# Kernel optimization log

Hardware: AMD Instinct MI355X
Metric: run time of the kernel (lower is better)

## Reference

```python
import jax, jax.numpy as jnp
import numpy as np
import math

N_FREQS = 32
MARGIN = 0.1
CHOUT = 270
POS_DIM = 2 * N_FREQS ** 2  # 2048


def fourier_emb(positions):
    # positions: [..., 2] in [0, 1]
    width = 1.0 + 2.0 * MARGIN
    p = (positions + MARGIN) / width
    f = jnp.arange(N_FREQS, dtype=p.dtype)
    two_pi = 2.0 * math.pi
    # phase[..., i, j] = 2*pi*(x*i + y*j)  -> flatten to [..., F*F]
    phase = two_pi * (p[..., 0][..., None, None] * f[:, None]
                      + p[..., 1][..., None, None] * f[None, :])
    phase = phase.reshape(*phase.shape[:-2], N_FREQS * N_FREQS)
    return jnp.concatenate([jnp.sin(phase), jnp.cos(phase)], axis=-1)  # [..., 2F^2]


def setup_inputs() -> dict:
    key = jax.random.key(0)
    k1, k2, k3 = jax.random.split(key, 3)
    B, C, T = 32, 273, 3000
    brain_data = jax.random.normal(k1, (B, C, T), dtype=jnp.float32)
    channel_layout = jax.random.uniform(k2, (B, C, 2), dtype=jnp.float32)
    heads = jax.random.normal(k3, (CHOUT, POS_DIM), dtype=jnp.float32) / POS_DIM ** 0.5
    return {"brain_data": brain_data, "channel_layout": channel_layout, "heads": heads}


def reference(brain_data, channel_layout, heads):
    # Eval mode: all channels valid, no dropout mask, zero score offset.
    emb = fourier_emb(channel_layout)                      # [B, C, D]
    scores = jnp.einsum('bcd,od->boc', emb, heads)         # [B, O, C]
    weights = jax.nn.softmax(scores, axis=-1)              # softmax over channels
    out = jnp.einsum('bct,boc->bot', brain_data, weights)  # [B, O, T]
    return out
```

## Files before the change

### kernel.cpp

```cpp
#include <hip/hip_runtime.h>
#include <hip/hip_bf16.h>
#include <hip/hip_fp16.h>

#define NB 32
#define NC 273
#define NT 3000
#define NO 270
#define ND 2048
#define CP 288

typedef _Float16 f16x8 __attribute__((ext_vector_type(8)));
typedef float f32x4 __attribute__((ext_vector_type(4)));

#define S_OFF 55296000UL
#define W_OFF 64730880UL
#define H_OFF 69707520UL

__device__ __forceinline__ unsigned short f2h_bits(float f) {
  _Float16 h = (_Float16)f;
  unsigned short u;
  __builtin_memcpy(&u, &h, 2);
  return u;
}

__global__ void heads_cvt_kernel(const float* __restrict__ heads,
                                 _Float16* __restrict__ hh) {
  const size_t idx = ((size_t)blockIdx.x * 256 + threadIdx.x) * 8;
  const float4 a = *reinterpret_cast<const float4*>(heads + idx);
  const float4 c = *reinterpret_cast<const float4*>(heads + idx + 4);
  f16x8 v;
  v[0] = (_Float16)a.x; v[1] = (_Float16)a.y; v[2] = (_Float16)a.z; v[3] = (_Float16)a.w;
  v[4] = (_Float16)c.x; v[5] = (_Float16)c.y; v[6] = (_Float16)c.z; v[7] = (_Float16)c.w;
  *reinterpret_cast<f16x8*>(hh + idx) = v;
}

__global__ void scores_kernel(const _Float16* __restrict__ hh,
                              const float* __restrict__ layout,
                              float* __restrict__ scores) {
  __shared__ _Float16 As[64][72];
  __shared__ _Float16 Bs[64][72];
  const int gid = blockIdx.x;
  const int tid = threadIdx.x;
  const int b = gid / 25;
  const int rem = gid % 25;
  const int o0 = (rem / 5) * 64;
  const int c0 = (rem % 5) * 64;
  const int lane = tid & 63, w = tid >> 6;
  const int wm = (w >> 1) * 32, wn = (w & 1) * 32;
  const int ln = lane & 15, quad = lane >> 4;
  const int sr = tid >> 2;
  const int sk = (tid & 3) * 16;

  const int ch = c0 + sr;
  float px = 0.f, py = 0.f;
  if (ch < NC) {
    const float inv = 1.0f / 1.2f;
    const float* lp = layout + ((size_t)b * NC + ch) * 2;
    px = (lp[0] + 0.1f) * inv;
    py = (lp[1] + 0.1f) * inv;
  }

  f32x4 acc[2][2] = {};

  for (int k0 = 0; k0 < ND; k0 += 64) {
    {
      const int o = o0 + sr;
      uint4 u0 = {0, 0, 0, 0}, u1 = {0, 0, 0, 0};
      if (o < NO) {
        const uint4* p = reinterpret_cast<const uint4*>(hh + (size_t)o * ND + k0 + sk);
        u0 = p[0]; u1 = p[1];
      }
      *reinterpret_cast<uint4*>(&As[sr][sk]) = u0;
      *reinterpret_cast<uint4*>(&As[sr][sk + 8]) = u1;
    }
    {
      const int kg = k0 + sk;
      const int dd = kg & 1023;
      const float base = px * (float)(dd >> 5) + py * (float)(dd & 31)
                       + ((kg < 1024) ? 0.0f : 0.25f);
      f16x8 h0, h1;
#pragma unroll
      for (int s = 0; s < 8; ++s) {
        float ph = base + py * (float)s;
        ph -= floorf(ph);
        h0[s] = (_Float16)__builtin_amdgcn_sinf(ph);
      }
#pragma unroll
      for (int s = 0; s < 8; ++s) {
        float ph = base + py * (float)(s + 8);
        ph -= floorf(ph);
        h1[s] = (_Float16)__builtin_amdgcn_sinf(ph);
      }
      *reinterpret_cast<f16x8*>(&Bs[sr][sk]) = h0;
      *reinterpret_cast<f16x8*>(&Bs[sr][sk + 8]) = h1;
    }
    __syncthreads();
#pragma unroll
    for (int ks = 0; ks < 64; ks += 32) {
      const int kf = ks + quad * 8;
      const f16x8 a0 = *reinterpret_cast<const f16x8*>(&As[wm + ln][kf]);
      const f16x8 a1 = *reinterpret_cast<const f16x8*>(&As[wm + 16 + ln][kf]);
      const f16x8 b0 = *reinterpret_cast<const f16x8*>(&Bs[wn + ln][kf]);
      const f16x8 b1 = *reinterpret_cast<const f16x8*>(&Bs[wn + 16 + ln][kf]);
      acc[0][0] = __builtin_amdgcn_mfma_f32_16x16x32_f16(a0, b0, acc[0][0], 0, 0, 0);
      acc[0][1] = __builtin_amdgcn_mfma_f32_16x16x32_f16(a0, b1, acc[0][1], 0, 0, 0);
      acc[1][0] = __builtin_amdgcn_mfma_f32_16x16x32_f16(a1, b0, acc[1][0], 0, 0, 0);
      acc[1][1] = __builtin_amdgcn_mfma_f32_16x16x32_f16(a1, b1, acc[1][1], 0, 0, 0);
    }
    __syncthreads();
  }

  float* sB = scores + (size_t)b * NO * NC;
#pragma unroll
  for (int i = 0; i < 2; ++i) {
    const int ob = o0 + wm + 16 * i + quad * 4;
#pragma unroll
    for (int j = 0; j < 2; ++j) {
      const int cc = c0 + wn + 16 * j + ln;
      if (cc >= NC) continue;
#pragma unroll
      for (int r = 0; r < 4; ++r) {
        const int o = ob + r;
        if (o < NO) sB[(size_t)o * NC + cc] = acc[i][j][r];
      }
    }
  }
}

__global__ void softmax_kernel(const float* __restrict__ sc,
                               _Float16* __restrict__ wq) {
  const int row = blockIdx.x * 4 + (threadIdx.x >> 6);
  const int lane = threadIdx.x & 63;
  const float* p = sc + (size_t)row * NC;
  _Float16* q = wq + (size_t)row * CP;
  float v[5];
  float m = -3.0e38f;
#pragma unroll
  for (int k = 0; k < 5; ++k) {
    const int c = lane + k * 64;
    v[k] = (c < NC) ? p[c] : -3.0e38f;
    m = fmaxf(m, v[k]);
  }
#pragma unroll
  for (int off = 32; off > 0; off >>= 1) m = fmaxf(m, __shfl_xor(m, off));
  float s = 0.f;
#pragma unroll
  for (int k = 0; k < 5; ++k) {
    v[k] = expf(v[k] - m);
    s += v[k];
  }
#pragma unroll
  for (int off = 32; off > 0; off >>= 1) s += __shfl_xor(s, off);
  const float r = 1.0f / s;
#pragma unroll
  for (int k = 0; k < 5; ++k) {
    const int c = lane + k * 64;
    if (c < NC) q[c] = (_Float16)(v[k] * r);
    else if (c < CP) q[c] = (_Float16)0.f;
  }
}

__global__ __launch_bounds__(256, 2) void out_kernel(
    const _Float16* __restrict__ wq,
    const float* __restrict__ brain,
    float* __restrict__ out) {
  __shared__ float raw[2][32][68];
  const int b = blockIdx.y;
  const int t0 = blockIdx.x * 64;
  const int tid = threadIdx.x;
  const int lane = tid & 63, w = tid >> 6;
  const int om = (w >> 1) * 32, tn = (w & 1) * 32;
  const int ln = lane & 15, quad = lane >> 4;

  const _Float16* Wb = wq + (size_t)b * NO * CP;

  const int cl = tid >> 3;
  const int tq = (tid & 7) * 4;
  const int tb = t0 + tq;
  const int wsw = (cl >> 3) << 4;
  const int ws0 = tq ^ wsw;
  const int ws1 = (tq + 32) ^ wsw;

  const int rc0 = (tn + ln) ^ (quad << 4);
  const int rc1 = (tn + 16 + ln) ^ (quad << 4);

  auto load_chunk = [&](int ci, float4& v0, float4& v1) {
    float4 z = {0.f, 0.f, 0.f, 0.f};
    v0 = z; v1 = z;
    const int c = ci * 32 + cl;
    if (c < NC) {
      const float* src = brain + ((size_t)b * NC + c) * NT + tb;
      if (tb + 35 < NT) {
        v0 = *reinterpret_cast<const float4*>(src);
        v1 = *reinterpret_cast<const float4*>(src + 32);
      } else {
        if (tb + 0 < NT) v0.x = src[0];
        if (tb + 1 < NT) v0.y = src[1];
        if (tb + 2 < NT) v0.z = src[2];
        if (tb + 3 < NT) v0.w = src[3];
        if (tb + 32 < NT) v1.x = src[32];
        if (tb + 33 < NT) v1.y = src[33];
        if (tb + 34 < NT) v1.z = src[34];
        if (tb + 35 < NT) v1.w = src[35];
      }
    }
  };

  auto store_raw = [&](int buf, const float4& v0, const float4& v1) {
    *reinterpret_cast<float4*>(&raw[buf][cl][ws0]) = v0;
    *reinterpret_cast<float4*>(&raw[buf][cl][ws1]) = v1;
  };

  auto load_a = [&](int s, f16x8 (&a)[10]) {
    const int kcol = s * 32 + quad * 8;
#pragma unroll
    for (int ot = 0; ot < 5; ++ot) {
      int r0 = ot * 64 + om + ln;      if (r0 > NO - 1) r0 = NO - 1;
      int r1 = ot * 64 + om + 16 + ln; if (r1 > NO - 1) r1 = NO - 1;
      a[2 * ot]     = *reinterpret_cast<const f16x8*>(Wb + (size_t)r0 * CP + kcol);
      a[2 * ot + 1] = *reinterpret_cast<const f16x8*>(Wb + (size_t)r1 * CP + kcol);
    }
  };

  f32x4 acc[5][2][2] = {};

  auto do_mfma = [&](const f16x8 (&a)[10], f16x8 b0, f16x8 b1) {
#pragma unroll
    for (int ot = 0; ot < 5; ++ot) {
      acc[ot][0][0] = __builtin_amdgcn_mfma_f32_16x16x32_f16(a[2*ot],   b0, acc[ot][0][0], 0, 0, 0);
      acc[ot][0][1] = __builtin_amdgcn_mfma_f32_16x16x32_f16(a[2*ot],   b1, acc[ot][0][1], 0, 0, 0);
      acc[ot][1][0] = __builtin_amdgcn_mfma_f32_16x16x32_f16(a[2*ot+1], b0, acc[ot][1][0], 0, 0, 0);
      acc[ot][1][1] = __builtin_amdgcn_mfma_f32_16x16x32_f16(a[2*ot+1], b1, acc[ot][1][1], 0, 0, 0);
    }
  };

  f16x8 aE[10], aO[10];
  float4 rA0, rA1, rB0, rB1;

  load_chunk(0, rA0, rA1);
  load_a(0, aE);
  load_chunk(1, rB0, rB1);
  store_raw(0, rA0, rA1);
  load_chunk(2, rA0, rA1);
  asm volatile("s_waitcnt lgkmcnt(0)" ::: "memory");
  __builtin_amdgcn_sched_barrier(0);
  __builtin_amdgcn_s_barrier();

#pragma unroll
  for (int s = 0; s < 9; ++s) {
    if (s < 8) {
      if (((s + 1) & 1) == 0) load_a(s + 1, aE); else load_a(s + 1, aO);
    }
    if (s < 8) {
      if (((s + 1) & 1) == 0) {
        store_raw(0, rA0, rA1);
        if (s < 6) load_chunk(s + 3, rA0, rA1);
      } else {
        store_raw(1, rB0, rB1);
        if (s < 6) load_chunk(s + 3, rB0, rB1);
      }
    }
    f16x8 b0, b1;
    {
      const float* rb = &raw[s & 1][0][0];
#pragma unroll
      for (int j = 0; j < 8; ++j) {
        const int row = quad * 8 + j;
        b0[j] = (_Float16)rb[row * 68 + rc0];
        b1[j] = (_Float16)rb[row * 68 + rc1];
      }
    }
    if (s < 8) {
      asm volatile("s_waitcnt lgkmcnt(0)" ::: "memory");
      __builtin_amdgcn_sched_barrier(0);
      __builtin_amdgcn_s_barrier();
    }
    if ((s & 1) == 0) do_mfma(aE, b0, b1); else do_mfma(aO, b0, b1);
  }

  float* oB = out + (size_t)b * NO * NT;
#pragma unroll
  for (int ot = 0; ot < 5; ++ot) {
#pragma unroll
    for (int i = 0; i < 2; ++i) {
      const int ob = ot * 64 + om + 16 * i + quad * 4;
#pragma unroll
      for (int j = 0; j < 2; ++j) {
        const int t = t0 + tn + 16 * j + ln;
        if (t >= NT) continue;
#pragma unroll
        for (int r = 0; r < 4; ++r) {
          const int o = ob + r;
          if (o < NO) oB[(size_t)o * NT + t] = acc[ot][i][j][r];
        }
      }
    }
  }
}

extern "C" void kernel_launch(void* const* d_in, const int* in_sizes, int n_in,
                              void* d_out, int out_size, void* d_ws, size_t ws_size,
                              hipStream_t stream) {
  const float* brain = (const float*)d_in[0];
  const float* layout = (const float*)d_in[1];
  const float* heads = (const float*)d_in[2];
  for (int i = 0; i < n_in; ++i) {
    if (in_sizes[i] == NB * NC * NT) brain = (const float*)d_in[i];
    else if (in_sizes[i] == NB * NC * 2) layout = (const float*)d_in[i];
    else if (in_sizes[i] == NO * ND) heads = (const float*)d_in[i];
  }
  float* out = (float*)d_out;

  float* scores = (float*)((char*)d_ws + S_OFF);
  _Float16* wq = (_Float16*)((char*)d_ws + W_OFF);
  _Float16* hh = (_Float16*)((char*)d_ws + H_OFF);

  heads_cvt_kernel<<<NO, 256, 0, stream>>>(heads, hh);
  scores_kernel<<<800, 256, 0, stream>>>(hh, layout, scores);
  softmax_kernel<<<(NB * NO) / 4, 256, 0, stream>>>(scores, wq);
  out_kernel<<<dim3(47, NB), 256, 0, stream>>>(wq, brain, out);
}
```

Baseline: 290.4 us.

## Stage full brain tile into LDS via direct global-to-LDS loads, drop pipeline

Replaces the double-buffered register-staged pipeline for the brain tile with a single bulk prefetch of all 288x64 floats into shared memory using global_load_lds (direct global-to-LDS DMA) with an XOR swizzle. The last channel is handled separately and the padding rows are zeroed. After one barrier, the MFMA loop reads from LDS with no per-step barriers. This removes register staging and per-chunk syncs. In exchange, LDS use rises to about 72KB per block, which may cut occupancy, and all loads must land before any compute can start.

```diff
diff --git a/kernel.cpp b/kernel.cpp
--- a/kernel.cpp
+++ b/kernel.cpp
@@ -15,13 +15,6 @@
 #define S_OFF 55296000UL
 #define W_OFF 64730880UL
 #define H_OFF 69707520UL
-
-__device__ __forceinline__ unsigned short f2h_bits(float f) {
-  _Float16 h = (_Float16)f;
-  unsigned short u;
-  __builtin_memcpy(&u, &h, 2);
-  return u;
-}
 
 __global__ void heads_cvt_kernel(const float* __restrict__ heads,
                                  _Float16* __restrict__ hh) {
@@ -164,7 +157,7 @@
     const _Float16* __restrict__ wq,
     const float* __restrict__ brain,
     float* __restrict__ out) {
-  __shared__ float raw[2][32][68];
+  __shared__ float Bs[CP * 64];
   const int b = blockIdx.y;
   const int t0 = blockIdx.x * 64;
   const int tid = threadIdx.x;
@@ -174,43 +167,6 @@
 
   const _Float16* Wb = wq + (size_t)b * NO * CP;
 
-  const int cl = tid >> 3;
-  const int tq = (tid & 7) * 4;
-  const int tb = t0 + tq;
-  const int wsw = (cl >> 3) << 4;
-  const int ws0 = tq ^ wsw;
-  const int ws1 = (tq + 32) ^ wsw;
-
-  const int rc0 = (tn + ln) ^ (quad << 4);
-  const int rc1 = (tn + 16 + ln) ^ (quad << 4);
-
-  auto load_chunk = [&](int ci, float4& v0, float4& v1) {
-    float4 z = {0.f, 0.f, 0.f, 0.f};
-    v0 = z; v1 = z;
-    const int c = ci * 32 + cl;
-    if (c < NC) {
-      const float* src = brain + ((size_t)b * NC + c) * NT + tb;
-      if (tb + 35 < NT) {
-        v0 = *reinterpret_cast<const float4*>(src);
-        v1 = *reinterpret_cast<const float4*>(src + 32);
-      } else {
-        if (tb + 0 < NT) v0.x = src[0];
-        if (tb + 1 < NT) v0.y = src[1];
-        if (tb + 2 < NT) v0.z = src[2];
-        if (tb + 3 < NT) v0.w = src[3];
-        if (tb + 32 < NT) v1.x = src[32];
-        if (tb + 33 < NT) v1.y = src[33];
-        if (tb + 34 < NT) v1.z = src[34];
-        if (tb + 35 < NT) v1.w = src[35];
-      }
-    }
-  };
-
-  auto store_raw = [&](int buf, const float4& v0, const float4& v1) {
-    *reinterpret_cast<float4*>(&raw[buf][cl][ws0]) = v0;
-    *reinterpret_cast<float4*>(&raw[buf][cl][ws1]) = v1;
-  };
-
   auto load_a = [&](int s, f16x8 (&a)[10]) {
     const int kcol = s * 32 + quad * 8;
 #pragma unroll
@@ -222,6 +178,46 @@
     }
   };
 
+  f16x8 aE[10], aO[10];
+  load_a(0, aE);
+
+  {
+    const int g16 = tid & 15;
+    const int crow = tid >> 4;
+    const float* gb = brain + (size_t)b * NC * NT + t0;
+#pragma unroll
+    for (int p = 0; p < 17; ++p) {
+      const int c = p * 16 + crow;
+      const int qc = (c >> 3) & 3;
+      const float* gptr = gb + (size_t)c * NT + 4 * (g16 ^ (qc << 1));
+      __builtin_amdgcn_global_load_lds(
+          (const __attribute__((address_space(1))) void*)gptr,
+          (__attribute__((address_space(3))) void*)(Bs + p * 1024 + w * 256),
+          16, 0, 0);
+    }
+  }
+  if (tid < 16) {
+    const float* src = brain + ((size_t)b * NC + 272) * NT + t0;
+    const int toff = 4 * (tid ^ 4);
+    float4 v = {0.f, 0.f, 0.f, 0.f};
+    if (t0 + toff + 3 < NT) {
+      v = *reinterpret_cast<const float4*>(src + toff);
+    } else {
+      if (t0 + toff + 0 < NT) v.x = src[toff + 0];
+      if (t0 + toff + 1 < NT) v.y = src[toff + 1];
+      if (t0 + toff + 2 < NT) v.z = src[toff + 2];
+    }
+    *reinterpret_cast<float4*>(Bs + 272 * 64 + tid * 4) = v;
+  }
+  if (tid < 240) {
+    const float4 z = {0.f, 0.f, 0.f, 0.f};
+    *reinterpret_cast<float4*>(Bs + 273 * 64 + tid * 4) = z;
+  }
+  asm volatile("s_waitcnt vmcnt(0) lgkmcnt(0)" ::: "memory");
+  __syncthreads();
+
+  const int rc0 = (tn + ln) ^ (quad << 3);
+  const int rc1 = (tn + 16 + ln) ^ (quad << 3);
   f32x4 acc[5][2][2] = {};
 
   auto do_mfma = [&](const f16x8 (&a)[10], f16x8 b0, f16x8 b1) {
@@ -234,46 +230,17 @@
     }
   };
 
-  f16x8 aE[10], aO[10];
-  float4 rA0, rA1, rB0, rB1;
-
-  load_chunk(0, rA0, rA1);
-  load_a(0, aE);
-  load_chunk(1, rB0, rB1);
-  store_raw(0, rA0, rA1);
-  load_chunk(2, rA0, rA1);
-  asm volatile("s_waitcnt lgkmcnt(0)" ::: "memory");
-  __builtin_amdgcn_sched_barrier(0);
-  __builtin_amdgcn_s_barrier();
-
 #pragma unroll
   for (int s = 0; s < 9; ++s) {
     if (s < 8) {
       if (((s + 1) & 1) == 0) load_a(s + 1, aE); else load_a(s + 1, aO);
     }
-    if (s < 8) {
-      if (((s + 1) & 1) == 0) {
-        store_raw(0, rA0, rA1);
-        if (s < 6) load_chunk(s + 3, rA0, rA1);
-      } else {
-        store_raw(1, rB0, rB1);
-        if (s < 6) load_chunk(s + 3, rB0, rB1);
-      }
-    }
     f16x8 b0, b1;
-    {
-      const float* rb = &raw[s & 1][0][0];
-#pragma unroll
-      for (int j = 0; j < 8; ++j) {
-        const int row = quad * 8 + j;
-        b0[j] = (_Float16)rb[row * 68 + rc0];
-        b1[j] = (_Float16)rb[row * 68 + rc1];
-      }
-    }
-    if (s < 8) {
-      asm volatile("s_waitcnt lgkmcnt(0)" ::: "memory");
-      __builtin_amdgcn_sched_barrier(0);
-      __builtin_amdgcn_s_barrier();
+#pragma unroll
+    for (int j = 0; j < 8; ++j) {
+      const int c = s * 32 + quad * 8 + j;
+      b0[j] = (_Float16)Bs[c * 64 + rc0];
+      b1[j] = (_Float16)Bs[c * 64 + rc1];
     }
     if ((s & 1) == 0) do_mfma(aE, b0, b1); else do_mfma(aO, b0, b1);
   }
```

Result: no change. 286.3 us (-1.4%).
